# Kernel tuning notes

Hardware: AMD Instinct MI355X
Metric: run time of the kernel (lower is better)

## Reference

```python
import jax, jax.numpy as jnp
import numpy as np

CHANNELS = 1024
N_HEADS = 16
N_EMBD = 512
H_DIM = CHANNELS // N_HEADS


def setup_inputs() -> dict:
    key = jax.random.key(0)
    ks = jax.random.split(key, 10)
    b, hw = 16, 4096
    s = 0.02
    return {
        "x": jax.random.normal(ks[0], (b, hw, CHANNELS), dtype=jnp.float32),
        "p": jax.random.normal(ks[1], (b, 77, N_EMBD), dtype=jnp.float32),
        "Wq": jax.random.normal(ks[2], (CHANNELS, CHANNELS), dtype=jnp.float32) * s,
        "bq": jnp.zeros((CHANNELS,), dtype=jnp.float32),
        "Wk": jax.random.normal(ks[3], (N_EMBD, CHANNELS), dtype=jnp.float32) * s,
        "bk": jnp.zeros((CHANNELS,), dtype=jnp.float32),
        "Wv": jax.random.normal(ks[4], (N_EMBD, CHANNELS), dtype=jnp.float32) * s,
        "bv": jnp.zeros((CHANNELS,), dtype=jnp.float32),
        "Ww": jax.random.normal(ks[5], (CHANNELS, CHANNELS), dtype=jnp.float32) * s,
        "bw": jnp.zeros((CHANNELS,), dtype=jnp.float32),
    }


def reference(x, p, Wq, bq, Wk, bk, Wv, bv, Ww, bw):
    b, hw, c = x.shape
    # Linear projections (torch Linear: y = x @ W^T + b; here weights stored as (in, out))
    q = x @ Wq + bq                      # (b, hw, c)
    k = p @ Wk + bk                      # (b, 77, c)
    v = p @ Wv + bv                      # (b, 77, c)
    q = q.reshape(b, hw, N_HEADS, H_DIM)
    k = k.reshape(b, 77, N_HEADS, H_DIM)
    v = v.reshape(b, 77, N_HEADS, H_DIM)
    scale = 1.0 / jnp.sqrt(jnp.asarray(H_DIM, dtype=x.dtype))
    # scores: (b, heads, hw, 77)
    scores = jnp.einsum("bqhd,bkhd->bhqk", q, k) * scale
    attn = jax.nn.softmax(scores, axis=-1)
    out = jnp.einsum("bhqk,bkhd->bqhd", attn, v).reshape(b, hw, c)
    return out @ Ww + bw
```

## Files before the change

### kernel.cpp

```cpp
#include <hip/hip_runtime.h>
#include <cstdint>
#include <type_traits>

typedef uint16_t u16;
typedef uint32_t u32;
typedef __attribute__((ext_vector_type(4))) float f32x4;
typedef __attribute__((ext_vector_type(8))) __bf16 vbf8;
typedef __attribute__((ext_vector_type(8))) short vs8;

template <typename T, typename = void>
struct CanMfma : std::false_type {};
template <typename T>
struct CanMfma<T, std::void_t<decltype(__builtin_amdgcn_mfma_f32_16x16x32_bf16(
    std::declval<T>(), std::declval<T>(), std::declval<f32x4>(), 0, 0, 0))>>
    : std::true_type {};
typedef std::conditional_t<CanMfma<vbf8>::value, vbf8, vs8> frag_t;

__device__ __forceinline__ f32x4 mfma_bf16(frag_t a, frag_t b, f32x4 c) {
  return __builtin_amdgcn_mfma_f32_16x16x32_bf16(a, b, c, 0, 0, 0);
}

__device__ __forceinline__ u16 f2bf(float f) {
  u32 u = __builtin_bit_cast(u32, f);
  u32 r = (u + 0x7FFFu + ((u >> 16) & 1u)) >> 16;
  return (u16)r;
}

__device__ __forceinline__ void gload_lds16(const void* g, void* l) {
  __builtin_amdgcn_global_load_lds(
      (const __attribute__((address_space(1))) void*)g,
      (__attribute__((address_space(3))) void*)l, 16, 0, 0);
}

__global__ __launch_bounds__(256) void cast_f32_bf16(
    const float* __restrict__ in, u16* __restrict__ out, int n8) {
  int i = blockIdx.x * 256 + threadIdx.x;
  const int stride = gridDim.x * 256;
  for (; i < n8; i += stride) {
    const float4 a  = ((const float4*)in)[(size_t)i * 2];
    const float4 b2 = ((const float4*)in)[(size_t)i * 2 + 1];
    uint4 o;
    o.x = (u32)f2bf(a.x)  | ((u32)f2bf(a.y)  << 16);
    o.y = (u32)f2bf(a.z)  | ((u32)f2bf(a.w)  << 16);
    o.z = (u32)f2bf(b2.x) | ((u32)f2bf(b2.y) << 16);
    o.w = (u32)f2bf(b2.z) | ((u32)f2bf(b2.w) << 16);
    ((uint4*)out)[(size_t)i] = o;
  }
}

__global__ __launch_bounds__(256) void transpose_cast(
    const float* __restrict__ in, u16* __restrict__ out, int K, int N) {
  __shared__ float tile[32][33];
  const int k0 = blockIdx.x * 32, n0 = blockIdx.y * 32;
  const int tr = threadIdx.x >> 5, tc = threadIdx.x & 31;
#pragma unroll
  for (int i = 0; i < 4; ++i)
    tile[tr + i * 8][tc] = in[(size_t)(k0 + tr + i * 8) * N + (n0 + tc)];
  __syncthreads();
#pragma unroll
  for (int i = 0; i < 4; ++i)
    out[(size_t)(n0 + tr + i * 8) * K + (k0 + tc)] = f2bf(tile[tc][tr + i * 8]);
}

template <bool OUT_BF16>
__global__ __launch_bounds__(256) void gemm_bt(
    const u16* __restrict__ A, const u16* __restrict__ Bt,
    const float* __restrict__ bias, void* __restrict__ Cout,
    int M, int N, int K, int Mtiles, int Ntiles) {
  __shared__ char Al[2][128 * 32 * 2];
  __shared__ char Bl[2][128 * 32 * 2];

  const int nwg = Mtiles * Ntiles;
  int bid = (int)blockIdx.x;
  bid = (bid & 7) * (nwg >> 3) + (bid >> 3);
  const int mt = bid / Ntiles, nt = bid % Ntiles;
  const int m0 = mt * 128, n0 = nt * 128;

  const int tid = (int)threadIdx.x;
  const int lane = tid & 63;
  const int wv = tid >> 6;
  const int wm = wv & 1, wn = wv >> 1;
  const int lr = lane & 15, lg = lane >> 4;
  const int rsub = lane >> 2;
  const int slot = lane & 3;
  const int rb0 = n0 + rsub;

  auto stage = [&](int buf, int t) {
    const int k0 = t << 5;
#pragma unroll
    for (int c = 0; c < 2; ++c) {
      const int ci = c * 4 + wv;
      int rra = m0 + ci * 16 + rsub;
      if (rra >= M) rra = M - 1;
      gload_lds16(A + (size_t)rra * K + k0 + slot * 8, Al[buf] + ci * 1024);
      const int rrb = rb0 + ci * 16;
      gload_lds16(Bt + (size_t)rrb * K + k0 + slot * 8, Bl[buf] + ci * 1024);
    }
  };

  f32x4 zero4 = {0.f, 0.f, 0.f, 0.f};
  f32x4 acc[4][4];
#pragma unroll
  for (int i = 0; i < 4; ++i)
#pragma unroll
    for (int j = 0; j < 4; ++j) acc[i][j] = zero4;

  const int nk = K >> 5;
  int cur = 0;
  stage(0, 0);
  __syncthreads();

  for (int t = 0; t < nk; ++t) {
    if (t + 1 < nk) stage(cur ^ 1, t + 1);
    frag_t af[4], bf[4];
#pragma unroll
    for (int i = 0; i < 4; ++i) {
      af[i] = *(const frag_t*)(Al[cur] + (wm * 64 + i * 16 + lr) * 64 + lg * 16);
      bf[i] = *(const frag_t*)(Bl[cur] + (wn * 64 + i * 16 + lr) * 64 + lg * 16);
    }
#pragma unroll
    for (int i = 0; i < 4; ++i)
#pragma unroll
      for (int j = 0; j < 4; ++j)
        acc[i][j] = mfma_bf16(af[i], bf[j], acc[i][j]);
    __syncthreads();
    cur ^= 1;
  }

#pragma unroll
  for (int j = 0; j < 4; ++j) {
    const int col = n0 + wn * 64 + j * 16 + lr;
    const float bv = bias[col];
#pragma unroll
    for (int i = 0; i < 4; ++i) {
      const int rbase = m0 + wm * 64 + i * 16 + lg * 4;
#pragma unroll
      for (int r = 0; r < 4; ++r) {
        const int row = rbase + r;
        const float val = acc[i][j][r] + bv;
        if constexpr (OUT_BF16) {
          u32 me = f2bf(val);
          u32 other = __shfl_xor(me, 1);
          if ((lane & 1) == 0 && row < M) {
            *(u32*)((u16*)Cout + (size_t)row * N + col) = me | (other << 16);
          }
        } else {
          if (row < M) ((float*)Cout)[(size_t)row * N + col] = val;
        }
      }
    }
  }
}

template <bool OUT_BF16>
__global__ __launch_bounds__(512) void gemm256(
    const u16* __restrict__ A, const u16* __restrict__ Bt,
    const float* __restrict__ bias, void* __restrict__ Cout,
    int M, int N, int K) {
  __shared__ u16 Al[2][256 * 64];
  __shared__ u16 Bl[2][256 * 64];

  const int Ntiles = N >> 8;
  const int nwg = (M >> 8) * Ntiles;
  int bid = (int)blockIdx.x;
  bid = (bid & 7) * (nwg >> 3) + (bid >> 3);
  const int mt = bid / Ntiles, ntl = bid % Ntiles;
  const int m0 = mt << 8, n0 = ntl << 8;

  const int tid = (int)threadIdx.x;
  const int lane = tid & 63;
  const int wid = tid >> 6;
  const int wm = wid >> 2, wn = wid & 3;
  const int lr = lane & 15, lg = lane >> 4;
  const int lrx = lr & 7;

  const int chunk = wid * 2;
  const int srow = lane >> 3;
  const int sslot = (lane & 7) ^ srow;
  const u16* Abase = A + (size_t)(m0 + chunk * 8 + srow) * K + sslot * 8;
  const u16* Bbase = Bt + (size_t)(n0 + chunk * 8 + srow) * K + sslot * 8;
  const int ldsChunkByte = (chunk * 8) * 128;

  auto stA = [&](u16* dst, int h, int t) {
    const u16* g = Abase + (size_t)(h << 7) * K + (t << 6);
    char* l = (char*)dst + (h << 14) + ldsChunkByte;
    gload_lds16(g, l);
    gload_lds16(g + ((size_t)K << 3), l + 1024);
  };
  auto stB = [&](u16* dst, int h, int t) {
    const u16* g = Bbase + (size_t)(h << 7) * K + (t << 6);
    char* l = (char*)dst + (h << 14) + ldsChunkByte;
    gload_lds16(g, l);
    gload_lds16(g + ((size_t)K << 3), l + 1024);
  };

  auto ldsF = [&](const u16* base, int row, int ks) -> frag_t {
    return *(const frag_t*)(base + (size_t)row * 64 + ((((ks) << 2) + lg) ^ lrx) * 8);
  };

  f32x4 zero4 = {0.f, 0.f, 0.f, 0.f};
  f32x4 acc[8][4];
#pragma unroll
  for (int i = 0; i < 8; ++i)
#pragma unroll
    for (int j = 0; j < 4; ++j) acc[i][j] = zero4;

  const int nt = K >> 6;
  const int ar0 = wm * 128 + lr;
  const int br0 = wn * 64 + lr;

  auto tileStep = [&](const u16* al, const u16* bl, u16* adst, u16* bdst,
                      int tA, int tB, bool onA, bool onB, int vm) {
    frag_t a[4][2], b0[2][2], b1[2][2];
#pragma unroll
    for (int i = 0; i < 4; ++i) {
      a[i][0] = ldsF(al, ar0 + i * 16, 0);
      a[i][1] = ldsF(al, ar0 + i * 16, 1);
    }
#pragma unroll
    for (int j = 0; j < 2; ++j) {
      b0[j][0] = ldsF(bl, br0 + j * 16, 0);
      b0[j][1] = ldsF(bl, br0 + j * 16, 1);
    }
    if (onA) stA(adst, 0, tA);
    __builtin_amdgcn_s_barrier();
    __builtin_amdgcn_s_setprio(1);
#pragma unroll
    for (int i = 0; i < 4; ++i)
#pragma unroll
      for (int j = 0; j < 2; ++j) {
        acc[i][j] = mfma_bf16(a[i][0], b0[j][0], acc[i][j]);
        acc[i][j] = mfma_bf16(a[i][1], b0[j][1], acc[i][j]);
      }
    __builtin_amdgcn_s_setprio(0);
    __builtin_amdgcn_s_barrier();
#pragma unroll
    for (int j = 0; j < 2; ++j) {
      b1[j][0] = ldsF(bl, br0 + 32 + j * 16, 0);
      b1[j][1] = ldsF(bl, br0 + 32 + j * 16, 1);
    }
    if (onA) stA(adst, 1, tA);
    __builtin_amdgcn_s_barrier();
    __builtin_amdgcn_s_setprio(1);
#pragma unroll
    for (int i = 0; i < 4; ++i)
#pragma unroll
      for (int j = 0; j < 2; ++j) {
        acc[i][2 + j] = mfma_bf16(a[i][0], b1[j][0], acc[i][2 + j]);
        acc[i][2 + j] = mfma_bf16(a[i][1], b1[j][1], acc[i][2 + j]);
      }
    __builtin_amdgcn_s_setprio(0);
    __builtin_amdgcn_s_barrier();
#pragma unroll
    for (int i = 0; i < 4; ++i) {
      a[i][0] = ldsF(al, ar0 + 64 + i * 16, 0);
      a[i][1] = ldsF(al, ar0 + 64 + i * 16, 1);
    }
    if (onB) stB(bdst, 0, tB);
    __builtin_amdgcn_s_barrier();
    __builtin_amdgcn_s_setprio(1);
#pragma unroll
    for (int i = 0; i < 4; ++i)
#pragma unroll
      for (int j = 0; j < 2; ++j) {
        acc[4 + i][2 + j] = mfma_bf16(a[i][0], b1[j][0], acc[4 + i][2 + j]);
        acc[4 + i][2 + j] = mfma_bf16(a[i][1], b1[j][1], acc[4 + i][2 + j]);
      }
    __builtin_amdgcn_s_setprio(0);
    __builtin_amdgcn_s_barrier();
    if (onB) stB(bdst, 1, tB);
    __builtin_amdgcn_s_barrier();
    __builtin_amdgcn_s_setprio(1);
#pragma unroll
    for (int i = 0; i < 4; ++i)
#pragma unroll
      for (int j = 0; j < 2; ++j) {
        acc[4 + i][j] = mfma_bf16(a[i][0], b0[j][0], acc[4 + i][j]);
        acc[4 + i][j] = mfma_bf16(a[i][1], b0[j][1], acc[4 + i][j]);
      }
    __builtin_amdgcn_s_setprio(0);
    if (vm == 4)
      asm volatile("s_waitcnt vmcnt(4)" ::: "memory");
    else if (vm == 0)
      asm volatile("s_waitcnt vmcnt(0)" ::: "memory");
    __builtin_amdgcn_s_barrier();
  };

  stA(&Al[0][0], 0, 0);
  stA(&Al[0][0], 1, 0);
  stB(&Bl[0][0], 0, 0);
  stB(&Bl[0][0], 1, 0);
  stB(&Bl[1][0], 0, 1);
  stB(&Bl[1][0], 1, 1);
  asm volatile("s_waitcnt vmcnt(4)" ::: "memory");
  __builtin_amdgcn_s_barrier();

  for (int t = 0; t + 2 < nt; t += 2) {
    tileStep(&Al[0][0], &Bl[0][0], &Al[1][0], &Bl[0][0], t + 1, t + 2, true, true, 4);
    tileStep(&Al[1][0], &Bl[1][0], &Al[0][0], &Bl[1][0], t + 2, t + 3,
             true, t + 3 < nt, (t + 3 < nt) ? 4 : 0);
  }
  tileStep(&Al[0][0], &Bl[0][0], &Al[1][0], &Bl[0][0], nt - 1, nt, true, false, 0);
  tileStep(&Al[1][0], &Bl[1][0], &Al[0][0], &Bl[1][0], nt, nt, false, false, -1);

#pragma unroll
  for (int bj = 0; bj < 4; ++bj) {
    const int col = n0 + wn * 64 + (bj >> 1) * 32 + (bj & 1) * 16 + lr;
    const float bv = bias[col];
#pragma unroll
    for (int ai = 0; ai < 8; ++ai) {
      const int rbase = m0 + wm * 128 + (ai >> 2) * 64 + (ai & 3) * 16 + lg * 4;
#pragma unroll
      for (int rr = 0; rr < 4; ++rr) {
        const float val = acc[ai][bj][rr] + bv;
        if constexpr (OUT_BF16) {
          u32 me = f2bf(val);
          u32 other = __shfl_xor(me, 1);
          if ((lane & 1) == 0) {
            *(u32*)((u16*)Cout + (size_t)(rbase + rr) * N + col) = me | (other << 16);
          }
        } else {
          ((float*)Cout)[(size_t)(rbase + rr) * N + col] = val;
        }
      }
    }
  }
}

__global__ __launch_bounds__(256) void attn_kernel(
    const u16* __restrict__ Q, const u16* __restrict__ K,
    const u16* __restrict__ V, u16* __restrict__ O) {
  __shared__ u16 Kl[96][72];
  __shared__ u16 Vt[64][104];

  const int bid = blockIdx.x;
  const int qt = bid & 63;
  const int h = (bid >> 6) & 15;
  const int b = bid >> 10;
  const int tid = threadIdx.x;

#pragma unroll
  for (int it = 0; it < 3; ++it) {
    const int idx = tid + it * 256;
    const int key = idx >> 3, s = idx & 7;
    uint4 val{0u, 0u, 0u, 0u};
    if (key < 77)
      val = *(const uint4*)(K + ((size_t)(b * 77 + key)) * 1024 + h * 64 + s * 8);
    *(uint4*)(&Kl[key][s * 8]) = val;
  }
#pragma unroll
  for (int it = 0; it < 3; ++it) {
    const int idx = tid + it * 256;
    if (idx < 616) {
      const int key = idx >> 3, s = idx & 7;
      const uint4 v4 =
          *(const uint4*)(V + ((size_t)(b * 77 + key)) * 1024 + h * 64 + s * 8);
      const u16* e = (const u16*)&v4;
#pragma unroll
      for (int j = 0; j < 8; ++j) Vt[s * 8 + j][key] = e[j];
    }
  }
#pragma unroll
  for (int it = 0; it < 5; ++it) {
    const int idx = tid + it * 256;
    if (idx < 1216) {
      const int d = idx / 19, kk = 77 + idx % 19;
      Vt[d][kk] = 0;
    }
  }
  __syncthreads();

  const int lane = tid & 63;
  const int wv = tid >> 6;
  const int lr = lane & 15;
  const int lg = lane >> 4;

  const size_t qrow = (size_t)(b * 4096 + qt * 64 + wv * 16 + lr) * 1024 + h * 64;
  frag_t qf[2];
#pragma unroll
  for (int ks = 0; ks < 2; ++ks)
    qf[ks] = *(const frag_t*)(Q + qrow + ks * 32 + lg * 8);

  f32x4 zero4 = {0.f, 0.f, 0.f, 0.f};
  f32x4 sa[5] = {zero4, zero4, zero4, zero4, zero4};
#pragma unroll
  for (int ks = 0; ks < 2; ++ks) {
#pragma unroll
    for (int kt = 0; kt < 5; ++kt) {
      frag_t kf = *(const frag_t*)(&Kl[kt * 16 + lr][ks * 32 + lg * 8]);
      sa[kt] = mfma_bf16(kf, qf[ks], sa[kt]);
    }
  }

  float p[5][4];
  float mx = -3.0e38f;
#pragma unroll
  for (int kt = 0; kt < 5; ++kt)
#pragma unroll
    for (int r = 0; r < 4; ++r) {
      const int key = kt * 16 + lg * 4 + r;
      float s = sa[kt][r] * 0.125f;
      if (key >= 77) s = -3.0e38f;
      p[kt][r] = s;
      mx = fmaxf(mx, s);
    }
  mx = fmaxf(mx, __shfl_xor(mx, 16));
  mx = fmaxf(mx, __shfl_xor(mx, 32));
  float sum = 0.f;
#pragma unroll
  for (int kt = 0; kt < 5; ++kt)
#pragma unroll
    for (int r = 0; r < 4; ++r) {
      const float e = __expf(p[kt][r] - mx);
      p[kt][r] = e;
      sum += e;
    }
  sum += __shfl_xor(sum, 16);
  sum += __shfl_xor(sum, 32);
  const float rden = 1.0f / sum;
#pragma unroll
  for (int kt = 0; kt < 5; ++kt)
#pragma unroll
    for (int r = 0; r < 4; ++r) p[kt][r] *= rden;

  union FP { frag_t v; u16 e[8]; };
  frag_t pa[3];
#pragma unroll
  for (int kb = 0; kb < 3; ++kb) {
    FP f;
#pragma unroll
    for (int j = 0; j < 8; ++j) {
      const int kt = 2 * kb + (j >> 2);
      f.e[j] = (kt < 5) ? f2bf(p[kt][j & 3]) : (u16)0;
    }
    pa[kb] = f.v;
  }

  f32x4 oa[4] = {zero4, zero4, zero4, zero4};
#pragma unroll
  for (int nt = 0; nt < 4; ++nt) {
    const int d = nt * 16 + lr;
#pragma unroll
    for (int kb = 0; kb < 3; ++kb) {
      const int key0 = kb * 32 + lg * 4;
      FP vb;
      *(uint2*)(&vb.e[0]) = *(const uint2*)(&Vt[d][key0]);
      *(uint2*)(&vb.e[4]) = *(const uint2*)(&Vt[d][key0 + 16]);
      oa[nt] = mfma_bf16(pa[kb], vb.v, oa[nt]);
    }
  }

#pragma unroll
  for (int nt = 0; nt < 4; ++nt)
#pragma unroll
    for (int r = 0; r < 4; ++r) {
      const int qr = wv * 16 + lg * 4 + r;
      u32 me = f2bf(oa[nt][r]);
      u32 other = __shfl_xor(me, 1);
      if ((lane & 1) == 0) {
        *(u32*)(O + ((size_t)(b * 4096 + qt * 64 + qr)) * 1024 + h * 64 +
                nt * 16 + lr) = me | (other << 16);
      }
    }
}

extern "C" void kernel_launch(void* const* d_in, const int* in_sizes, int n_in,
                              void* d_out, int out_size, void* d_ws, size_t ws_size,
                              hipStream_t stream) {
  const float* x  = (const float*)d_in[0];
  const float* p  = (const float*)d_in[1];
  const float* Wq = (const float*)d_in[2];
  const float* bq = (const float*)d_in[3];
  const float* Wk = (const float*)d_in[4];
  const float* bk = (const float*)d_in[5];
  const float* Wv = (const float*)d_in[6];
  const float* bv = (const float*)d_in[7];
  const float* Ww = (const float*)d_in[8];
  const float* bw = (const float*)d_in[9];

  char* ws = (char*)d_ws;
  if (ws_size < 281034752ULL) return;

  u16* x_bf = (u16*)(ws + 0);
  u16* q_bf = (u16*)(ws + 134217728);
  u16* wq_t = (u16*)(ws + 268435456);
  u16* ww_t = (u16*)(ws + 270532608);
  u16* wk_t = (u16*)(ws + 272629760);
  u16* wv_t = (u16*)(ws + 273678336);
  u16* p_bf = (u16*)(ws + 274726912);
  u16* k_bf = (u16*)(ws + 275988480);
  u16* v_bf = (u16*)(ws + 278511616);

  cast_f32_bf16<<<4096, 256, 0, stream>>>(x, x_bf, 8388608);
  cast_f32_bf16<<<308, 256, 0, stream>>>(p, p_bf, 78848);
  transpose_cast<<<dim3(32, 32), 256, 0, stream>>>(Wq, wq_t, 1024, 1024);
  transpose_cast<<<dim3(32, 32), 256, 0, stream>>>(Ww, ww_t, 1024, 1024);
  transpose_cast<<<dim3(16, 32), 256, 0, stream>>>(Wk, wk_t, 512, 1024);
  transpose_cast<<<dim3(16, 32), 256, 0, stream>>>(Wv, wv_t, 512, 1024);

  gemm_bt<true><<<80, 256, 0, stream>>>(p_bf, wk_t, bk, k_bf, 1232, 1024, 512, 10, 8);
  gemm_bt<true><<<80, 256, 0, stream>>>(p_bf, wv_t, bv, v_bf, 1232, 1024, 512, 10, 8);
  gemm256<true><<<1024, 512, 0, stream>>>(x_bf, wq_t, bq, q_bf, 65536, 1024, 1024);
  attn_kernel<<<16384, 256, 0, stream>>>(q_bf, k_bf, v_bf, x_bf);
  gemm256<false><<<1024, 512, 0, stream>>>(x_bf, ww_t, bw, d_out, 65536, 1024, 1024);
}
```

Before: 625.6 us.

## Restructure GEMM main loop to prefetch next tile's LDS fragments across steps

```diff
diff --git a/kernel.cpp b/kernel.cpp
--- a/kernel.cpp
+++ b/kernel.cpp
@@ -31,6 +31,9 @@
       (const __attribute__((address_space(1))) void*)g,
       (__attribute__((address_space(3))) void*)l, 16, 0, 0);
 }
+
+#define VMW(n) asm volatile("s_waitcnt vmcnt(" #n ")" ::: "memory")
+#define SB0() __builtin_amdgcn_sched_barrier(0)
 
 __global__ __launch_bounds__(256) void cast_f32_bf16(
     const float* __restrict__ in, u16* __restrict__ out, int n8) {
@@ -209,118 +212,115 @@
   const int ar0 = wm * 128 + lr;
   const int br0 = wn * 64 + lr;
 
-  auto tileStep = [&](const u16* al, const u16* bl, u16* adst, u16* bdst,
-                      int tA, int tB, bool onA, bool onB, int vm) {
-    frag_t a[4][2], b0[2][2], b1[2][2];
+  frag_t a0[4][2], a1[4][2], b0A[2][2], b0B[2][2], b1[2][2];
+
+  auto rdA0 = [&](const u16* al) {
 #pragma unroll
     for (int i = 0; i < 4; ++i) {
-      a[i][0] = ldsF(al, ar0 + i * 16, 0);
-      a[i][1] = ldsF(al, ar0 + i * 16, 1);
-    }
+      a0[i][0] = ldsF(al, ar0 + i * 16, 0);
+      a0[i][1] = ldsF(al, ar0 + i * 16, 1);
+    }
+  };
+  auto rdA1 = [&](const u16* al) {
+#pragma unroll
+    for (int i = 0; i < 4; ++i) {
+      a1[i][0] = ldsF(al, ar0 + 64 + i * 16, 0);
+      a1[i][1] = ldsF(al, ar0 + 64 + i * 16, 1);
+    }
+  };
+  auto rdB0 = [&](const u16* bl, frag_t (&d)[2][2]) {
 #pragma unroll
     for (int j = 0; j < 2; ++j) {
-      b0[j][0] = ldsF(bl, br0 + j * 16, 0);
-      b0[j][1] = ldsF(bl, br0 + j * 16, 1);
-    }
-    if (onA) stA(adst, 0, tA);
-    __builtin_amdgcn_s_barrier();
-    __builtin_amdgcn_s_setprio(1);
-#pragma unroll
-    for (int i = 0; i < 4; ++i)
-#pragma unroll
-      for (int j = 0; j < 2; ++j) {
-        acc[i][j] = mfma_bf16(a[i][0], b0[j][0], acc[i][j]);
-        acc[i][j] = mfma_bf16(a[i][1], b0[j][1], acc[i][j]);
-      }
-    __builtin_amdgcn_s_setprio(0);
-    __builtin_amdgcn_s_barrier();
+      d[j][0] = ldsF(bl, br0 + j * 16, 0);
+      d[j][1] = ldsF(bl, br0 + j * 16, 1);
+    }
+  };
+  auto rdB1 = [&](const u16* bl) {
 #pragma unroll
     for (int j = 0; j < 2; ++j) {
       b1[j][0] = ldsF(bl, br0 + 32 + j * 16, 0);
       b1[j][1] = ldsF(bl, br0 + 32 + j * 16, 1);
     }
-    if (onA) stA(adst, 1, tA);
-    __builtin_amdgcn_s_barrier();
+  };
+  auto mmaQ = [&](frag_t (&a)[4][2], frag_t (&b)[2][2], int io, int jo) {
     __builtin_amdgcn_s_setprio(1);
 #pragma unroll
     for (int i = 0; i < 4; ++i)
 #pragma unroll
       for (int j = 0; j < 2; ++j) {
-        acc[i][2 + j] = mfma_bf16(a[i][0], b1[j][0], acc[i][2 + j]);
-        acc[i][2 + j] = mfma_bf16(a[i][1], b1[j][1], acc[i][2 + j]);
+        acc[io + i][jo + j] = mfma_bf16(a[i][0], b[j][0], acc[io + i][jo + j]);
+        acc[io + i][jo + j] = mfma_bf16(a[i][1], b[j][1], acc[io + i][jo + j]);
       }
     __builtin_amdgcn_s_setprio(0);
+  };
+
+  auto tileStep = [&](const u16* al, const u16* bl, u16* alN, u16* blN,
+                      frag_t (&b0c)[2][2], frag_t (&b0n)[2][2], int tN,
+                      bool nl) {
+    if (nl) {
+      stB(blN, 0, tN); stB(blN, 1, tN);
+      stA(alN, 0, tN); stA(alN, 1, tN);
+    }
+    rdB1(bl);
+    SB0();
+    mmaQ(a0, b0c, 0, 0);
+    SB0();
     __builtin_amdgcn_s_barrier();
-#pragma unroll
-    for (int i = 0; i < 4; ++i) {
-      a[i][0] = ldsF(al, ar0 + 64 + i * 16, 0);
-      a[i][1] = ldsF(al, ar0 + 64 + i * 16, 1);
-    }
-    if (onB) stB(bdst, 0, tB);
+    rdA1(al);
+    SB0();
+    mmaQ(a0, b1, 0, 2);
+    SB0();
+    if (nl) VMW(4);
     __builtin_amdgcn_s_barrier();
-    __builtin_amdgcn_s_setprio(1);
-#pragma unroll
-    for (int i = 0; i < 4; ++i)
-#pragma unroll
-      for (int j = 0; j < 2; ++j) {
-        acc[4 + i][2 + j] = mfma_bf16(a[i][0], b1[j][0], acc[4 + i][2 + j]);
-        acc[4 + i][2 + j] = mfma_bf16(a[i][1], b1[j][1], acc[4 + i][2 + j]);
-      }
-    __builtin_amdgcn_s_setprio(0);
+    if (nl) rdB0(blN, b0n);
+    SB0();
+    mmaQ(a1, b1, 4, 2);
+    SB0();
+    if (nl) VMW(0);
     __builtin_amdgcn_s_barrier();
-    if (onB) stB(bdst, 1, tB);
+    if (nl) rdA0(alN);
+    SB0();
+    mmaQ(a1, b0c, 4, 0);
+    SB0();
     __builtin_amdgcn_s_barrier();
-    __builtin_amdgcn_s_setprio(1);
-#pragma unroll
-    for (int i = 0; i < 4; ++i)
-#pragma unroll
-      for (int j = 0; j < 2; ++j) {
-        acc[4 + i][j] = mfma_bf16(a[i][0], b0[j][0], acc[4 + i][j]);
-        acc[4 + i][j] = mfma_bf16(a[i][1], b0[j][1], acc[4 + i][j]);
-      }
-    __builtin_amdgcn_s_setprio(0);
-    if (vm == 4)
-      asm volatile("s_waitcnt vmcnt(4)" ::: "memory");
-    else if (vm == 0)
-      asm volatile("s_waitcnt vmcnt(0)" ::: "memory");
-    __builtin_amdgcn_s_barrier();
-  };
-
-  stA(&Al[0][0], 0, 0);
-  stA(&Al[0][0], 1, 0);
-  stB(&Bl[0][0], 0, 0);
-  stB(&Bl[0][0], 1, 0);
-  stB(&Bl[1][0], 0, 1);
-  stB(&Bl[1][0], 1, 1);
-  asm volatile("s_waitcnt vmcnt(4)" ::: "memory");
+  };
+
+  stB(&Bl[0][0], 0, 0); stB(&Bl[0][0], 1, 0);
+  stA(&Al[0][0], 0, 0); stA(&Al[0][0], 1, 0);
+  VMW(0);
   __builtin_amdgcn_s_barrier();
-
-  for (int t = 0; t + 2 < nt; t += 2) {
-    tileStep(&Al[0][0], &Bl[0][0], &Al[1][0], &Bl[0][0], t + 1, t + 2, true, true, 4);
-    tileStep(&Al[1][0], &Bl[1][0], &Al[0][0], &Bl[1][0], t + 2, t + 3,
-             true, t + 3 < nt, (t + 3 < nt) ? 4 : 0);
-  }
-  tileStep(&Al[0][0], &Bl[0][0], &Al[1][0], &Bl[0][0], nt - 1, nt, true, false, 0);
-  tileStep(&Al[1][0], &Bl[1][0], &Al[0][0], &Bl[1][0], nt, nt, false, false, -1);
-
-#pragma unroll
-  for (int bj = 0; bj < 4; ++bj) {
-    const int col = n0 + wn * 64 + (bj >> 1) * 32 + (bj & 1) * 16 + lr;
-    const float bv = bias[col];
-#pragma unroll
-    for (int ai = 0; ai < 8; ++ai) {
-      const int rbase = m0 + wm * 128 + (ai >> 2) * 64 + (ai & 3) * 16 + lg * 4;
-#pragma unroll
-      for (int rr = 0; rr < 4; ++rr) {
-        const float val = acc[ai][bj][rr] + bv;
+  rdA0(&Al[0][0]);
+  rdB0(&Bl[0][0], b0A);
+
+  for (int tt = 0; tt < nt; tt += 2) {
+    tileStep(&Al[0][0], &Bl[0][0], &Al[1][0], &Bl[1][0], b0A, b0B, tt + 1,
+             tt + 1 < nt);
+    tileStep(&Al[1][0], &Bl[1][0], &Al[0][0], &Bl[0][0], b0B, b0A, tt + 2,
+             tt + 2 < nt);
+  }
+
+  float bvv[4];
+#pragma unroll
+  for (int bj = 0; bj < 4; ++bj)
+    bvv[bj] = bias[n0 + wn * 64 + (bj >> 1) * 32 + (bj & 1) * 16 + lr];
+#pragma unroll
+  for (int ai = 0; ai < 8; ++ai) {
+    const int rbase = m0 + wm * 128 + (ai >> 2) * 64 + (ai & 3) * 16 + lg * 4;
+#pragma unroll
+    for (int rr = 0; rr < 4; ++rr) {
+      const int row = rbase + rr;
+#pragma unroll
+      for (int bj = 0; bj < 4; ++bj) {
+        const int col = n0 + wn * 64 + (bj >> 1) * 32 + (bj & 1) * 16 + lr;
+        const float val = acc[ai][bj][rr] + bvv[bj];
         if constexpr (OUT_BF16) {
           u32 me = f2bf(val);
           u32 other = __shfl_xor(me, 1);
           if ((lane & 1) == 0) {
-            *(u32*)((u16*)Cout + (size_t)(rbase + rr) * N + col) = me | (other << 16);
+            *(u32*)((u16*)Cout + (size_t)row * N + col) = me | (other << 16);
           }
         } else {
-          ((float*)Cout)[(size_t)(rbase + rr) * N + col] = val;
+          ((float*)Cout)[(size_t)row * N + col] = val;
         }
       }
     }
```

Measured after the change: 845.7 us. +35.2%, slower.
